# Kernel optimization log

Hardware: AMD Instinct MI355X
Metric: run time of the kernel (lower is better)

## Reference

```python
import jax, jax.numpy as jnp
import numpy as np

NX, T_IN, T_OUT = 256, 16, 128
STATE, PSIZE = 1, 4
WIDTH, DEPTH = 128, 4
BATCH = 4


def _build_edges(B):
    # Faithful vectorized replica of create_graph_structure (incl. the
    # batch-mixing .view(2,-1) on a (B,2,E) tensor).
    ng = NX * T_OUT
    # spatial edges: loops t outer, i inner, fwd/bwd interleaved
    a = (np.arange(T_OUT)[:, None] * NX + np.arange(NX - 1)[None, :]).reshape(-1)
    sp = np.stack([np.stack([a, a + 1], 1), np.stack([a + 1, a], 1)], 1).reshape(-1, 2)
    # temporal edges: loops x outer, t inner, fwd/bwd interleaved
    b = (np.arange(NX)[:, None] + np.arange(T_OUT - 1)[None, :] * NX).reshape(-1)
    tp = np.stack([np.stack([b, b + NX], 1), np.stack([b + NX, b], 1)], 1).reshape(-1, 2)
    base = np.concatenate([sp, tp], 0).T  # (2, E)
    ei = base[None, :, :] + (np.arange(B) * ng)[:, None, None]  # (B, 2, E)
    return ei.reshape(2, -1)  # row-major flatten, same as torch .view(2, -1)


def _layernorm(x, g, b, eps=1e-5):
    mu = x.mean(-1, keepdims=True)
    var = x.var(-1, keepdims=True)  # biased, same as torch LayerNorm
    return (x - mu) * jax.lax.rsqrt(var + eps) * g + b


def setup_inputs():
    key = jax.random.key(0)
    ks = jax.random.split(key, 8)
    d_in = STATE + PSIZE + 2
    return {
        "u0": jax.random.normal(ks[0], (BATCH, NX, T_IN, STATE), jnp.float32),
        "P": jax.random.normal(ks[1], (BATCH, PSIZE), jnp.float32),
        "W_in": jax.random.normal(ks[2], (d_in, WIDTH), jnp.float32) / np.sqrt(d_in),
        "b_in": jnp.zeros((WIDTH,), jnp.float32),
        "Wg": jax.random.normal(ks[3], (DEPTH, WIDTH, WIDTH), jnp.float32) / np.sqrt(WIDTH),
        "bg": jnp.zeros((DEPTH, WIDTH), jnp.float32),
        "gamma": jnp.ones((DEPTH, WIDTH), jnp.float32),
        "beta": jnp.zeros((DEPTH, WIDTH), jnp.float32),
        "W_out": jax.random.normal(ks[4], (WIDTH, STATE), jnp.float32) / np.sqrt(WIDTH),
        "b_out": jnp.zeros((STATE,), jnp.float32),
    }


def reference(u0, P, W_in, b_in, Wg, bg, gamma, beta, W_out, b_out):
    B = u0.shape[0]
    ng = NX * T_OUT
    N = B * ng

    ei = _build_edges(B)
    loops = np.arange(N)
    src = jnp.asarray(np.concatenate([ei[0], loops]))  # GCN adds self-loops
    dst = jnp.asarray(np.concatenate([ei[1], loops]))
    deg = jnp.zeros((N,), jnp.float32).at[dst].add(1.0)  # in-degree incl. self-loop
    dis = jnp.where(deg > 0, jax.lax.rsqrt(deg), 0.0)
    norm = (dis[src] * dis[dst])[:, None]  # symmetric GCN normalization

    # grid features flattened x-major (matches meshgrid 'ij' reshape(-1,1))
    xg = jnp.repeat(jnp.linspace(0.0, 1.0, NX), T_OUT)[None, :, None]
    tg = jnp.tile(jnp.linspace(0.0, 1.0, T_OUT), NX)[None, :, None]

    # bilinear resize (nx_in, T_in) -> (NX, T_OUT), align_corners=False semantics
    u0i = jax.image.resize(u0, (B, NX, T_OUT, STATE), "bilinear").reshape(B, ng, STATE)
    Pex = jnp.broadcast_to(P[:, None, :], (B, ng, PSIZE))
    feat = jnp.concatenate(
        [u0i, Pex, jnp.broadcast_to(xg, (B, ng, 1)), jnp.broadcast_to(tg, (B, ng, 1))], -1
    )
    x = (feat @ W_in + b_in).reshape(N, WIDTH)

    for l in range(DEPTH):
        h = x @ Wg[l]                      # GCNConv linear
        msg = h[src] * norm                # gather + normalize
        h = jax.ops.segment_sum(msg, dst, num_segments=N) + bg[l]  # scatter-add
        h = _layernorm(h, gamma[l], beta[l])
        x = jax.nn.relu(h + x)             # residual then ReLU

    out = x @ W_out + b_out
    return out.reshape(B, NX, T_OUT, STATE)
```

## Files before the change

kernel.cpp:

```cpp
#include <hip/hip_runtime.h>
#include <hip/hip_bf16.h>

#define NXX 256
#define NG 32768
#define WID 128
#define STRW 68

typedef short bf16x8 __attribute__((ext_vector_type(8)));
typedef float f32x4 __attribute__((ext_vector_type(4)));

__device__ __forceinline__ unsigned short rne_bf16(float x) {
    unsigned int u = __float_as_uint(x);
    return (unsigned short)((u + 0x7fffu + ((u >> 16) & 1u)) >> 16);
}

__global__ __launch_bounds__(64) void prep_kernel(
    const float* __restrict__ Wg, unsigned short* __restrict__ Bfrag) {
    const int e  = blockIdx.x;
    const int lv = threadIdx.x;
    const int l  = e >> 5;
    const int kc = (e >> 3) & 3;
    const int nt = e & 7;
    const int n  = nt * 16 + (lv & 15);
    const int kb = kc * 32 + ((lv >> 4) << 3);
#pragma unroll
    for (int j = 0; j < 8; ++j) {
        float v = Wg[(size_t)l * 16384 + (size_t)(kb + j) * WID + n];
        Bfrag[(size_t)e * 512 + lv * 8 + j] = rne_bf16(v);
    }
}

__device__ __forceinline__ unsigned int pack_bf2(float a, float b) {
    union { __hip_bfloat162 h2; unsigned int u; } cv;
    cv.h2 = __float22bfloat162_rn(make_float2(a, b));
    return cv.u;
}

__global__ __launch_bounds__(256) void fused_kernel(
    const float* __restrict__ u0, const float* __restrict__ P,
    const float* __restrict__ W_in, const float* __restrict__ b_in,
    const unsigned short* __restrict__ Bfrag,
    const float* __restrict__ bg, const float* __restrict__ gamma,
    const float* __restrict__ beta, const float* __restrict__ W_out,
    const float* __restrict__ b_out, float* __restrict__ out)
{
    __shared__ unsigned int XsH[8][16 * STRW];

    const int tid  = threadIdx.x;
    const int w    = tid >> 6;
    const int lane = tid & 63;
    const int l15  = lane & 15;
    const int lhi  = lane >> 4;

    const int blk  = blockIdx.x;
    const int b    = blk >> 9;
    const int ublk = (blk & 511) << 6;

    const int u  = ublk + 16 * w + l15;
    const int ix = u >> 7;
    const int t  = u & 127;

    float c1, c2;
    {
        int gi = u & 255, gt = u >> 8;
        int d  = (gi > 0) + (gi < 255) + (gt > 0) + (gt < 127);
        float deg = 2.f * (float)d + 1.f;
        c1 = 2.f * (float)d * rsqrtf(deg);
        c2 = 1.f / deg;
    }

    float featA[7], featB[7];
    {
        float s  = ((float)t + 0.5f) * 0.125f - 0.5f;
        float fs = floorf(s);
        int   t0 = (int)fs;
        float wt = s - fs;
        int t0c = t0 < 0 ? 0 : (t0 > 15 ? 15 : t0);
        int t1n = t0 + 1;
        int t1c = t1n < 0 ? 0 : (t1n > 15 ? 15 : t1n);
        const float* urA = u0 + ((size_t)b * NXX + ix) * 16;
        const float* urB = u0 + ((size_t)(b + 2) * NXX + ix) * 16;
        featA[0] = urA[t0c] * (1.f - wt) + urA[t1c] * wt;
        featB[0] = urB[t0c] * (1.f - wt) + urB[t1c] * wt;
#pragma unroll
        for (int f = 0; f < 4; ++f) {
            featA[1 + f] = P[b * 4 + f];
            featB[1 + f] = P[(b + 2) * 4 + f];
        }
        featA[5] = featB[5] = (float)ix * (1.f / 255.f);
        featA[6] = featB[6] = (float)t  * (1.f / 127.f);
    }

    float xr0[8][4], xr1[8][4];
#pragma unroll
    for (int nt = 0; nt < 8; ++nt) {
        const int c = nt * 16 + 4 * lhi;
        float4 bi4 = *(const float4*)(b_in + c);
        float4 wf[7];
#pragma unroll
        for (int f = 0; f < 7; ++f) wf[f] = *(const float4*)(W_in + f * WID + c);
#pragma unroll
        for (int r = 0; r < 4; ++r) {
            float a0 = ((const float*)&bi4)[r];
            float a1 = a0;
#pragma unroll
            for (int f = 0; f < 7; ++f) {
                float wv = ((const float*)&wf[f])[r];
                a0 = fmaf(featA[f], wv, a0);
                a1 = fmaf(featB[f], wv, a1);
            }
            xr0[nt][r] = a0;
            xr1[nt][r] = a1;
        }
    }

    unsigned int* Hrow0 = &XsH[2 * w][l15 * STRW];
    unsigned int* Hrow1 = &XsH[2 * w + 1][l15 * STRW];

    for (int l = 0; l < 4; ++l) {
#pragma unroll
        for (int nt = 0; nt < 8; ++nt) {
            unsigned int p0 = pack_bf2(xr0[nt][0], xr0[nt][1]);
            unsigned int p1 = pack_bf2(xr0[nt][2], xr0[nt][3]);
            *(uint2*)(Hrow0 + 8 * nt + 2 * lhi) = make_uint2(p0, p1);
            unsigned int q0 = pack_bf2(xr1[nt][0], xr1[nt][1]);
            unsigned int q1 = pack_bf2(xr1[nt][2], xr1[nt][3]);
            *(uint2*)(Hrow1 + 8 * nt + 2 * lhi) = make_uint2(q0, q1);
        }

        bf16x8 xh0[4], xh1[4];
#pragma unroll
        for (int kc = 0; kc < 4; ++kc) {
            xh0[kc] = *(const bf16x8*)(Hrow0 + 16 * kc + 4 * lhi);
            xh1[kc] = *(const bf16x8*)(Hrow1 + 16 * kc + 4 * lhi);
        }

        f32x4 acc0[8], acc1[8];
        const unsigned short* bp = Bfrag + (size_t)l * 16384 + lane * 8;
#pragma unroll
        for (int nt = 0; nt < 8; ++nt) {
            f32x4 a0 = {0.f, 0.f, 0.f, 0.f};
            f32x4 a1 = {0.f, 0.f, 0.f, 0.f};
#pragma unroll
            for (int kc = 0; kc < 4; ++kc) {
                bf16x8 bh = *(const bf16x8*)(bp + (kc * 8 + nt) * 512);
                a0 = __builtin_amdgcn_mfma_f32_16x16x32_bf16(bh, xh0[kc], a0, 0, 0, 0);
                a1 = __builtin_amdgcn_mfma_f32_16x16x32_bf16(bh, xh1[kc], a1, 0, 0, 0);
            }
            acc0[nt] = a0;
            acc1[nt] = a1;
        }

        float s0 = 0.f, q0 = 0.f, s1 = 0.f, q1 = 0.f;
#pragma unroll
        for (int nt = 0; nt < 8; ++nt) {
            float4 bg4 = *(const float4*)(bg + l * WID + nt * 16 + 4 * lhi);
#pragma unroll
            for (int r = 0; r < 4; ++r) {
                float bgr = ((const float*)&bg4)[r];
                float h0 = acc0[nt][r];
                float h1 = acc1[nt][r];
                float a0 = h0 + bgr;
                float a1 = fmaf(c1, h0, fmaf(c2, h1, bgr));
                acc0[nt][r] = a0;
                acc1[nt][r] = a1;
                s0 += a0;  q0 = fmaf(a0, a0, q0);
                s1 += a1;  q1 = fmaf(a1, a1, q1);
            }
        }
        s0 += __shfl_xor(s0, 16);  q0 += __shfl_xor(q0, 16);
        s1 += __shfl_xor(s1, 16);  q1 += __shfl_xor(q1, 16);
        s0 += __shfl_xor(s0, 32);  q0 += __shfl_xor(q0, 32);
        s1 += __shfl_xor(s1, 32);  q1 += __shfl_xor(q1, 32);
        float mu0 = s0 * (1.f / 128.f);
        float mu1 = s1 * (1.f / 128.f);
        float rs0 = rsqrtf(q0 * (1.f / 128.f) - mu0 * mu0 + 1e-5f);
        float rs1 = rsqrtf(q1 * (1.f / 128.f) - mu1 * mu1 + 1e-5f);
#pragma unroll
        for (int nt = 0; nt < 8; ++nt) {
            const int c = nt * 16 + 4 * lhi;
            float4 g4 = *(const float4*)(gamma + l * WID + c);
            float4 e4 = *(const float4*)(beta  + l * WID + c);
#pragma unroll
            for (int r = 0; r < 4; ++r) {
                float gv = ((const float*)&g4)[r];
                float ev = ((const float*)&e4)[r];
                float n0 = fmaf((acc0[nt][r] - mu0) * rs0, gv, ev);
                float n1 = fmaf((acc1[nt][r] - mu1) * rs1, gv, ev);
                xr0[nt][r] = fmaxf(n0 + xr0[nt][r], 0.f);
                xr1[nt][r] = fmaxf(n1 + xr1[nt][r], 0.f);
            }
        }
    }

    float p0 = 0.f, p1 = 0.f;
#pragma unroll
    for (int nt = 0; nt < 8; ++nt) {
        float4 wo4 = *(const float4*)(W_out + nt * 16 + 4 * lhi);
#pragma unroll
        for (int r = 0; r < 4; ++r) {
            float wv = ((const float*)&wo4)[r];
            p0 = fmaf(xr0[nt][r], wv, p0);
            p1 = fmaf(xr1[nt][r], wv, p1);
        }
    }
    p0 += __shfl_xor(p0, 16);  p1 += __shfl_xor(p1, 16);
    p0 += __shfl_xor(p0, 32);  p1 += __shfl_xor(p1, 32);
    if (lhi == 0) {
        float bo = b_out[0];
        out[(size_t)b * NG + u]       = p0 + bo;
        out[(size_t)(b + 2) * NG + u] = p1 + bo;
    }
}

extern "C" void kernel_launch(void* const* d_in, const int* in_sizes, int n_in,
                              void* d_out, int out_size, void* d_ws, size_t ws_size,
                              hipStream_t stream) {
    const float* u0    = (const float*)d_in[0];
    const float* P     = (const float*)d_in[1];
    const float* W_in  = (const float*)d_in[2];
    const float* b_in  = (const float*)d_in[3];
    const float* Wg    = (const float*)d_in[4];
    const float* bg    = (const float*)d_in[5];
    const float* gamma = (const float*)d_in[6];
    const float* beta  = (const float*)d_in[7];
    const float* W_out = (const float*)d_in[8];
    const float* b_out = (const float*)d_in[9];

    unsigned short* Bfrag = (unsigned short*)d_ws;

    prep_kernel<<<128, 64, 0, stream>>>(Wg, Bfrag);
    fused_kernel<<<1024, 256, 0, stream>>>(
        u0, P, W_in, b_in, Bfrag, bg, gamma, beta, W_out, b_out, (float*)d_out);
}
```

Baseline: 62.25 us.

## Permute weight K-order to feed MFMA from registers and stage weights in LDS

Result: slower. 102.8 us (+65.2%).

```diff
diff --git a/kernel.cpp b/kernel.cpp
--- a/kernel.cpp
+++ b/kernel.cpp
@@ -4,10 +4,10 @@
 #define NXX 256
 #define NG 32768
 #define WID 128
-#define STRW 68
 
 typedef short bf16x8 __attribute__((ext_vector_type(8)));
 typedef float f32x4 __attribute__((ext_vector_type(4)));
+typedef unsigned int u32x4 __attribute__((ext_vector_type(4)));
 
 __device__ __forceinline__ unsigned short rne_bf16(float x) {
     unsigned int u = __float_as_uint(x);
@@ -22,10 +22,11 @@
     const int kc = (e >> 3) & 3;
     const int nt = e & 7;
     const int n  = nt * 16 + (lv & 15);
-    const int kb = kc * 32 + ((lv >> 4) << 3);
+    const int g  = lv >> 4;
 #pragma unroll
     for (int j = 0; j < 8; ++j) {
-        float v = Wg[(size_t)l * 16384 + (size_t)(kb + j) * WID + n];
+        const int ch = kc * 32 + ((j >> 2) << 4) + (g << 2) + (j & 3);
+        float v = Wg[(size_t)l * 16384 + (size_t)ch * WID + n];
         Bfrag[(size_t)e * 512 + lv * 8 + j] = rne_bf16(v);
     }
 }
@@ -35,6 +36,8 @@
     cv.h2 = __float22bfloat162_rn(make_float2(a, b));
     return cv.u;
 }
+
+union fragu { bf16x8 f; u32x4 u; };
 
 __global__ __launch_bounds__(256) void fused_kernel(
     const float* __restrict__ u0, const float* __restrict__ P,
@@ -44,7 +47,7 @@
     const float* __restrict__ beta, const float* __restrict__ W_out,
     const float* __restrict__ b_out, float* __restrict__ out)
 {
-    __shared__ unsigned int XsH[8][16 * STRW];
+    __shared__ unsigned short Wlds[2 * 16384];
 
     const int tid  = threadIdx.x;
     const int w    = tid >> 6;
@@ -59,6 +62,11 @@
     const int u  = ublk + 16 * w + l15;
     const int ix = u >> 7;
     const int t  = u & 127;
+
+    const uint4* gW = (const uint4*)Bfrag;
+    uint4 stg[8];
+#pragma unroll
+    for (int it = 0; it < 8; ++it) stg[it] = gW[tid + it * 256];
 
     float c1, c2;
     {
@@ -114,38 +122,48 @@
         }
     }
 
-    unsigned int* Hrow0 = &XsH[2 * w][l15 * STRW];
-    unsigned int* Hrow1 = &XsH[2 * w + 1][l15 * STRW];
+    {
+        char* swr = (char*)Wlds + tid * 16;
+#pragma unroll
+        for (int it = 0; it < 8; ++it)
+            *(uint4*)(swr + it * 4096) = stg[it];
+    }
+    __syncthreads();
+
+    const char* wbase = (const char*)Wlds + lane * 16;
 
     for (int l = 0; l < 4; ++l) {
-#pragma unroll
-        for (int nt = 0; nt < 8; ++nt) {
-            unsigned int p0 = pack_bf2(xr0[nt][0], xr0[nt][1]);
-            unsigned int p1 = pack_bf2(xr0[nt][2], xr0[nt][3]);
-            *(uint2*)(Hrow0 + 8 * nt + 2 * lhi) = make_uint2(p0, p1);
-            unsigned int q0 = pack_bf2(xr1[nt][0], xr1[nt][1]);
-            unsigned int q1 = pack_bf2(xr1[nt][2], xr1[nt][3]);
-            *(uint2*)(Hrow1 + 8 * nt + 2 * lhi) = make_uint2(q0, q1);
-        }
-
-        bf16x8 xh0[4], xh1[4];
+        const int cur = (l & 1) << 15;
+
+        if (l < 3) {
+#pragma unroll
+            for (int it = 0; it < 8; ++it)
+                stg[it] = gW[(l + 1) * 2048 + tid + it * 256];
+        }
+
+        fragu xh0[4], xh1[4];
 #pragma unroll
         for (int kc = 0; kc < 4; ++kc) {
-            xh0[kc] = *(const bf16x8*)(Hrow0 + 16 * kc + 4 * lhi);
-            xh1[kc] = *(const bf16x8*)(Hrow1 + 16 * kc + 4 * lhi);
+            xh0[kc].u = (u32x4){pack_bf2(xr0[2 * kc][0],     xr0[2 * kc][1]),
+                                pack_bf2(xr0[2 * kc][2],     xr0[2 * kc][3]),
+                                pack_bf2(xr0[2 * kc + 1][0], xr0[2 * kc + 1][1]),
+                                pack_bf2(xr0[2 * kc + 1][2], xr0[2 * kc + 1][3])};
+            xh1[kc].u = (u32x4){pack_bf2(xr1[2 * kc][0],     xr1[2 * kc][1]),
+                                pack_bf2(xr1[2 * kc][2],     xr1[2 * kc][3]),
+                                pack_bf2(xr1[2 * kc + 1][0], xr1[2 * kc + 1][1]),
+                                pack_bf2(xr1[2 * kc + 1][2], xr1[2 * kc + 1][3])};
         }
 
         f32x4 acc0[8], acc1[8];
-        const unsigned short* bp = Bfrag + (size_t)l * 16384 + lane * 8;
 #pragma unroll
         for (int nt = 0; nt < 8; ++nt) {
             f32x4 a0 = {0.f, 0.f, 0.f, 0.f};
             f32x4 a1 = {0.f, 0.f, 0.f, 0.f};
 #pragma unroll
             for (int kc = 0; kc < 4; ++kc) {
-                bf16x8 bh = *(const bf16x8*)(bp + (kc * 8 + nt) * 512);
-                a0 = __builtin_amdgcn_mfma_f32_16x16x32_bf16(bh, xh0[kc], a0, 0, 0, 0);
-                a1 = __builtin_amdgcn_mfma_f32_16x16x32_bf16(bh, xh1[kc], a1, 0, 0, 0);
+                bf16x8 bh = *(const bf16x8*)(wbase + cur + (kc * 8 + nt) * 1024);
+                a0 = __builtin_amdgcn_mfma_f32_16x16x32_bf16(bh, xh0[kc].f, a0, 0, 0, 0);
+                a1 = __builtin_amdgcn_mfma_f32_16x16x32_bf16(bh, xh1[kc].f, a1, 0, 0, 0);
             }
             acc0[nt] = a0;
             acc1[nt] = a1;
@@ -190,6 +208,15 @@
                 xr0[nt][r] = fmaxf(n0 + xr0[nt][r], 0.f);
                 xr1[nt][r] = fmaxf(n1 + xr1[nt][r], 0.f);
             }
+        }
+
+        if (l < 3) {
+            const int nxt = ((l + 1) & 1) << 15;
+            char* swr = (char*)Wlds + nxt + tid * 16;
+#pragma unroll
+            for (int it = 0; it < 8; ++it)
+                *(uint4*)(swr + it * 4096) = stg[it];
+            __syncthreads();
         }
     }
 
```
